# Kernel tuning notes

Measured on AMD Instinct MI355X. Metric: run time of the kernel, lower is better.

Reference implementation:

```python
import jax, jax.numpy as jnp
import numpy as np

EPS = 1e-8
TEMP = 0.1
D, H = 512, 256  # hidden_dim, hidden_dim // 2
BI, R = 64, 36   # images, regions
BC, W = 64, 50   # captions, words


def _l2norm(x):
    n = jnp.linalg.norm(x, axis=-1, keepdims=True)
    return x / jnp.maximum(n, 1e-12)


def _gate(x, w1, b1, w2, b2):
    h = jax.nn.relu(x @ w1 + b1)
    return jax.nn.sigmoid(h @ w2 + b2)  # [..., 1]


def setup_inputs() -> dict:
    key = jax.random.key(0)
    ks = jax.random.split(key, 12)
    imgs = jax.random.normal(ks[0], (BI, R, D), dtype=jnp.float32)
    caps = jax.random.normal(ks[1], (BC, W, D), dtype=jnp.float32)
    img_lens = jax.random.randint(ks[2], (BI,), 1, R + 1).at[0].set(R).astype(jnp.int32)
    cap_lens = jax.random.randint(ks[3], (BC,), 1, W + 1).at[0].set(W).astype(jnp.int32)
    s = 0.02
    return {
        'imgs': imgs, 'caps': caps,
        'soft_w1': jax.random.normal(ks[4], (D, H), dtype=jnp.float32) * s,
        'soft_b1': jnp.zeros((H,), dtype=jnp.float32),
        'soft_w2': jax.random.normal(ks[5], (H, 1), dtype=jnp.float32) * s,
        'soft_b2': jnp.zeros((1,), dtype=jnp.float32),
        'hard_w1': jax.random.normal(ks[6], (D, H), dtype=jnp.float32) * s,
        'hard_b1': jnp.zeros((H,), dtype=jnp.float32),
        'hard_w2': jax.random.normal(ks[7], (H, 1), dtype=jnp.float32) * s,
        'hard_b2': jnp.zeros((1,), dtype=jnp.float32),
        'img_lens': img_lens, 'cap_lens': cap_lens,
    }


def reference(imgs, caps, soft_w1, soft_b1, soft_w2, soft_b2,
              hard_w1, hard_b1, hard_w2, hard_b2, img_lens, cap_lens):
    Bi, R_, D_ = imgs.shape
    Bc, W_, _ = caps.shape
    img_mask = jnp.arange(R_)[None, :] < img_lens[:, None]  # [Bi,R]
    cap_mask = jnp.arange(W_)[None, :] < cap_lens[:, None]  # [Bc,W]
    mask = img_mask[:, None, :, None] & cap_mask[None, :, None, :]  # [Bi,Bc,R,W]

    # fine-grained region-word similarities
    sims = jnp.einsum('ird,cwd->icrw', imgs, caps)

    # hard (top-1) attention: argmax over words, one-hot scatter, re-masked
    idx = jnp.argmax(jnp.where(mask, sims, -1.0), axis=-1)  # [Bi,Bc,R]
    hard_attn = jnp.where(mask, jax.nn.one_hot(idx, W_, dtype=sims.dtype), 0.0)

    # soft attention with temperature and mask
    soft = jax.nn.softmax(jnp.where(mask, sims / TEMP, -jnp.inf), axis=-1)
    soft_attn = jnp.where(mask, soft, 0.0)

    hard_wc = jnp.einsum('icrw,cwd->icrd', hard_attn, caps)
    soft_wc = jnp.einsum('icrw,cwd->icrd', soft_attn, caps)

    # per-region learned gates, normalized to sum ~1
    sg = _gate(imgs, soft_w1, soft_b1, soft_w2, soft_b2)  # [Bi,R,1]
    hg = _gate(imgs, hard_w1, hard_b1, hard_w2, hard_b2)  # [Bi,R,1]
    tot = sg + hg + EPS
    sg = (sg / tot)[:, None, :, :]  # [Bi,1,R,1]
    hg = (hg / tot)[:, None, :, :]

    mixed = sg * soft_wc + hg * hard_wc  # [Bi,Bc,R,D]

    # per-pair, per-region cosine similarity
    out = jnp.einsum('ird,icrd->icr', _l2norm(imgs), _l2norm(mixed))
    return jnp.where(img_mask[:, None, :], out, -1.0)  # [Bi,Bc,R]
```

## Files before the change

kernel.cpp:

```cpp
#include <hip/hip_runtime.h>
#include <math.h>

#define BI 64
#define RR 36
#define BC 64
#define WW 50
#define DD 512
#define HH 256
#define CST 132

typedef _Float16 f16x8 __attribute__((ext_vector_type(8)));
typedef _Float16 f16x4 __attribute__((ext_vector_type(4)));
typedef float    f32x4 __attribute__((ext_vector_type(4)));

__device__ __forceinline__ float wave_sum(float v){
  #pragma unroll
  for (int off=32; off>0; off>>=1) v += __shfl_xor(v, off, 64);
  return v;
}
__device__ __forceinline__ float wave_max(float v){
  #pragma unroll
  for (int off=32; off>0; off>>=1) v = fmaxf(v, __shfl_xor(v, off, 64));
  return v;
}

__device__ __forceinline__ void gl_lds16(const _Float16* g, _Float16* l){
  __builtin_amdgcn_global_load_lds(
      (const __attribute__((address_space(1))) unsigned int*)g,
      (__attribute__((address_space(3))) unsigned int*)l, 16, 0, 0);
}

__global__ __launch_bounds__(256) void prepgram_kernel(
    const float* __restrict__ imgs, const float* __restrict__ caps,
    const float* __restrict__ sw1, const float* __restrict__ hw1,
    _Float16* __restrict__ Ah, _Float16* __restrict__ Al,
    _Float16* __restrict__ Bh, _Float16* __restrict__ Bl,
    float* __restrict__ G, _Float16* __restrict__ Gfrag)
{
  __shared__ __align__(16) float smem[WW*CST + 1024];
  if (blockIdx.x < 1504){
    int u = blockIdx.x*256 + threadIdx.x;
    _Float16 *dh, *dl; int idx;
    if (u < 144*1024){ idx = u;            dh = Ah; dl = Al; }
    else             { idx = u - 144*1024; dh = Bh; dl = Bl; }
    const int tile = idx >> 10, rem = idx & 1023, ks = rem >> 6, lane = rem & 63;
    const int k0 = ks*32 + (lane >> 4)*8;
    f16x8 hv, lv;
    if (u < 144*1024 || tile < 200){
      const float* src = (u < 144*1024) ? imgs : caps;
      const int m = tile*16 + (lane & 15);
      const float* p = src + (size_t)m*DD + k0;
      #pragma unroll
      for (int j=0;j<8;j++){
        float a = p[j];
        _Float16 h = (_Float16)a;
        hv[j] = h;
        lv[j] = (_Float16)((a - (float)h) * 2048.0f);
      }
    } else {
      const int n = (tile-200)*16 + (lane & 15);
      const float* src = (n < HH) ? (sw1 + n) : (hw1 + n - HH);
      #pragma unroll
      for (int j=0;j<8;j++){
        float a = src[(size_t)(k0+j)*HH];
        _Float16 h = (_Float16)a;
        hv[j] = h;
        lv[j] = (_Float16)((a - (float)h) * 2048.0f);
      }
    }
    *(f16x8*)(dh + (size_t)idx*8) = hv;
    *(f16x8*)(dl + (size_t)idx*8) = lv;
  } else {
    float* cs = smem;
    float* Gt = smem + WW*CST;
    const int bxg  = blockIdx.x - 1504;
    const int c    = bxg >> 2;
    const int tile = bxg & 3;
    const int w0   = tile*16;
    const int nw   = (tile==3) ? 2 : 16;
    const int t=threadIdx.x, lane=t&63, wv=t>>6;
    const int wl = lane < WW ? lane : WW-1;
    float acc[4]={0.f,0.f,0.f,0.f};
    for (int k0=0;k0<DD;k0+=128){
      __syncthreads();
      for (int n=t;n<WW*32;n+=256){
        int row=n>>5, c4=(n&31)*4;
        *(float4*)&cs[row*CST+c4] = *(const float4*)(caps + ((size_t)c*WW+row)*DD + k0 + c4);
      }
      __syncthreads();
      for (int k=0;k<128;k+=4){
        float4 cv = *(const float4*)&cs[wl*CST+k];
        #pragma unroll
        for (int q=0;q<4;q++){
          int lw = wv + q*4;
          if (lw < nw){
            float4 bv = *(const float4*)&cs[(w0+lw)*CST+k];
            acc[q]=fmaf(bv.x,cv.x,acc[q]); acc[q]=fmaf(bv.y,cv.y,acc[q]);
            acc[q]=fmaf(bv.z,cv.z,acc[q]); acc[q]=fmaf(bv.w,cv.w,acc[q]);
          }
        }
      }
    }
    for (int n=t;n<1024;n+=256) Gt[n]=0.f;
    __syncthreads();
    if (lane < WW){
      #pragma unroll
      for (int q=0;q<4;q++){
        int lw = wv + q*4;
        if (lw < nw){
          G[(size_t)c*WW*WW + (w0+lw)*WW + lane] = acc[q];
          Gt[lw*64 + lane] = acc[q];
        }
      }
    }
    __syncthreads();
    {
      int flat = t*4;
      int ks = flat>>9, L=(flat>>3)&63, j0=flat&7;
      const bool ones = (tile==3) && ((L&15)==2);
      f16x4 v;
      #pragma unroll
      for (int e=0;e<4;e++)
        v[e] = ones ? (_Float16)1.0f
                    : (_Float16)Gt[(L&15)*64 + ks*32 + ((L>>4)<<3) + j0 + e];
      *(f16x4*)&Gfrag[(size_t)c*4096 + (tile*2+ks)*512 + L*8 + j0] = v;
    }
  }
}

__global__ __launch_bounds__(256, 2) void sgemm_hgate_kernel(
    const _Float16* __restrict__ Ah, const _Float16* __restrict__ Al,
    const _Float16* __restrict__ Bh, const _Float16* __restrict__ Bl,
    float* __restrict__ Sp,
    const float* __restrict__ imgs,
    const float* __restrict__ sb1, const float* __restrict__ hb1,
    const float* __restrict__ sw2, const float* __restrict__ hw2,
    float* __restrict__ drawS, float* __restrict__ drawH,
    float* __restrict__ rnraw)
{
  __shared__ _Float16 lds[2*16384];
  const int t = threadIdx.x, lane = t & 63, wv = t >> 6;

  if (blockIdx.x >= 36){
    const int bx = blockIdx.x - 36;
    const int mb = bx % 18, nb = bx / 18;
    const int wm = wv & 1, wn = wv >> 1;

    f32x4 P[4][4], Q[4][4];
    #pragma unroll
    for (int a=0;a<4;a++)
      #pragma unroll
      for (int b=0;b<4;b++){ P[a][b]=(f32x4){0,0,0,0}; Q[a][b]=(f32x4){0,0,0,0}; }

    const _Float16* sbase = (wv==0)?Ah:(wv==1)?Al:(wv==2)?Bh:Bl;
    const size_t gtb = (size_t)((wv<2)? mb : nb)*8;
    _Float16* buf0 = lds + wv*4096;
    _Float16* buf1 = lds + 16384 + wv*4096;

    #pragma unroll
    for (int s=0;s<8;s++)
      gl_lds16(sbase + (((gtb+s)*16 + 0)*64 + lane)*8, buf0 + s*512);
    asm volatile("s_waitcnt vmcnt(0)" ::: "memory");
    __syncthreads();

    for (int ks=0; ks<16; ks++){
      if (ks < 15){
        _Float16* nb_ = ((ks+1) & 1) ? buf1 : buf0;
        #pragma unroll
        for (int s=0;s<8;s++)
          gl_lds16(sbase + (((gtb+s)*16 + (ks+1))*64 + lane)*8, nb_ + s*512);
      }

      const _Float16* L = lds + (ks & 1)*16384;
      f16x8 a_h[4], a_l[4], b_h[4], b_l[4];
      #pragma unroll
      for (int x=0;x<4;x++){
        a_h[x] = *(const f16x8*)&L[        (wm*4+x)*512 + lane*8];
        a_l[x] = *(const f16x8*)&L[ 4096 + (wm*4+x)*512 + lane*8];
        b_h[x] = *(const f16x8*)&L[ 8192 + (wn*4+x)*512 + lane*8];
        b_l[x] = *(const f16x8*)&L[12288 + (wn*4+x)*512 + lane*8];
      }
      #pragma unroll
      for (int mi=0;mi<4;mi++)
        #pragma unroll
        for (int ni=0;ni<4;ni++){
          P[mi][ni] = __builtin_amdgcn_mfma_f32_16x16x32_f16(a_h[mi], b_h[ni], P[mi][ni],0,0,0);
          Q[mi][ni] = __builtin_amdgcn_mfma_f32_16x16x32_f16(a_h[mi], b_l[ni], Q[mi][ni],0,0,0);
          Q[mi][ni] = __builtin_amdgcn_mfma_f32_16x16x32_f16(a_l[mi], b_h[ni], Q[mi][ni],0,0,0);
        }

      if (ks < 15)
        asm volatile("s_waitcnt vmcnt(0)" ::: "memory");
      __syncthreads();
    }

    const int r0 = mb*128 + wm*64 + ((lane>>4)<<2);
    const int c0 = nb*128 + wn*64 + (lane&15);
    size_t pr[16]; size_t pc[4];
    #pragma unroll
    for (int mi=0;mi<4;mi++)
      #pragma unroll
      for (int reg=0;reg<4;reg++){
        unsigned row = (unsigned)(r0 + mi*16 + reg);
        unsigned i = row / 36u, rr_ = row - i*36u;
        pr[mi*4+reg] = (size_t)i*115200u + (size_t)rr_*50u;
      }
    #pragma unroll
    for (int ni=0;ni<4;ni++){
      unsigned col = (unsigned)(c0 + ni*16);
      unsigned cc = col / 50u, w = col - cc*50u;
      pc[ni] = (size_t)cc*1800u + w;
    }
    #pragma unroll
    for (int mi=0;mi<4;mi++)
      #pragma unroll
      for (int ni=0;ni<4;ni++)
        #pragma unroll
        for (int reg=0;reg<4;reg++)
          Sp[pr[mi*4+reg] + pc[ni]] =
              P[mi][ni][reg] + Q[mi][ni][reg]*(1.0f/2048.0f);
    return;
  }

  const int mb = blockIdx.x >> 1;
  const int br = blockIdx.x & 1;
  const int wm = wv & 1, wn = wv >> 1;

  f32x4 P[4][8];
  #pragma unroll
  for (int a=0;a<4;a++)
    #pragma unroll
    for (int b=0;b<8;b++) P[a][b]=(f32x4){0,0,0,0};

  const _Float16* Bbase = Bh + (size_t)(200 + br*16)*8192;

  #pragma unroll
  for (int s=0;s<6;s++){
    const int u = wv*6 + s;
    const _Float16* src = (u < 8)
      ? (Ah    + ((size_t)((mb*8 + u)*16 + 0)*64 + lane)*8)
      : (Bbase + ((size_t)((u-8)  *16 + 0)*64 + lane)*8);
    _Float16* dst = (u < 8) ? (lds + u*512) : (lds + 4096 + (u-8)*512);
    gl_lds16(src, dst);
  }
  asm volatile("s_waitcnt vmcnt(0)" ::: "memory");
  __syncthreads();

  for (int ks=0; ks<16; ks++){
    if (ks < 15){
      _Float16* buf = lds + (((ks+1) & 1) ? 16384 : 0);
      #pragma unroll
      for (int s=0;s<6;s++){
        const int u = wv*6 + s;
        const _Float16* src = (u < 8)
          ? (Ah    + ((size_t)((mb*8 + u)*16 + (ks+1))*64 + lane)*8)
          : (Bbase + ((size_t)((u-8)  *16 + (ks+1))*64 + lane)*8);
        _Float16* dst = (u < 8) ? (buf + u*512) : (buf + 4096 + (u-8)*512);
        gl_lds16(src, dst);
      }
    }

    const _Float16* L = lds + (ks & 1)*16384;
    f16x8 a[4], b[8];
    #pragma unroll
    for (int x=0;x<4;x++)
      a[x] = *(const f16x8*)&L[(wm*4+x)*512 + lane*8];
    #pragma unroll
    for (int y=0;y<8;y++)
      b[y] = *(const f16x8*)&L[4096 + (wn*8+y)*512 + lane*8];
    #pragma unroll
    for (int mi=0;mi<4;mi++)
      #pragma unroll
      for (int ni=0;ni<8;ni++)
        P[mi][ni] = __builtin_amdgcn_mfma_f32_16x16x32_f16(a[mi], b[ni], P[mi][ni],0,0,0);

    if (ks < 15)
      asm volatile("s_waitcnt vmcnt(0)" ::: "memory");
    __syncthreads();
  }

  const float* b1 = br ? hb1 : sb1;
  const float* w2 = br ? hw2 : sw2;
  float bvv[8], wvv[8];
  #pragma unroll
  for (int ni=0;ni<8;ni++){
    const int cb = wn*128 + ni*16 + (lane&15);
    bvv[ni] = b1[cb]; wvv[ni] = w2[cb];
  }
  float contrib[16];
  #pragma unroll
  for (int mi=0;mi<4;mi++)
    #pragma unroll
    for (int reg=0;reg<4;reg++){
      float cacc = 0.f;
      #pragma unroll
      for (int ni=0;ni<8;ni++)
        cacc = fmaf(fmaxf(P[mi][ni][reg] + bvv[ni], 0.f), wvv[ni], cacc);
      #pragma unroll
      for (int off=1; off<16; off<<=1) cacc += __shfl_xor(cacc, off, 64);
      contrib[mi*4+reg] = cacc;
    }

  float* red = (float*)lds;
  if ((lane & 15) == 0){
    const int rbase = wm*64 + ((lane>>4)<<2);
    #pragma unroll
    for (int mi=0;mi<4;mi++)
      #pragma unroll
      for (int reg=0;reg<4;reg++)
        red[wn*128 + rbase + mi*16 + reg] = contrib[mi*4+reg];
  }
  __syncthreads();
  if (t < 128){
    float draw = red[t] + red[128 + t];
    (br ? drawH : drawS)[mb*128 + t] = draw;
  }

  if (br == 0){
    const int row = mb*128 + (t >> 1);
    const float* p = imgs + (size_t)row*DD + (t & 1)*256;
    float ss = 0.f;
    #pragma unroll
    for (int q=0;q<64;q++){
      float4 x = ((const float4*)p)[q];
      ss += x.x*x.x + x.y*x.y + x.z*x.z + x.w*x.w;
    }
    ss += __shfl_xor(ss, 1, 64);
    if ((t & 1) == 0) rnraw[row] = ss;
  }
}

__global__ __launch_bounds__(512) void epi_kernel(
    const float* __restrict__ Sp,
    const int* __restrict__ img_lens, const int* __restrict__ cap_lens,
    const float* __restrict__ drawS, const float* __restrict__ drawH,
    const float* __restrict__ rnraw,
    const float* __restrict__ G, const _Float16* __restrict__ Gfrag,
    const float* __restrict__ sb2, const float* __restrict__ hb2,
    float* __restrict__ out)
{
  __shared__ __align__(16) _Float16 sEp[48*72];
  __shared__ __align__(16) _Float16 sE2[48*72];
  __shared__ __align__(16) _Float16 sFp[48*72];
  __shared__ __align__(16) _Float16 sGf[4096];
  __shared__ float sTd[48];
  __shared__ float sTS[48];
  __shared__ float sGd[64];
  __shared__ float sAv[40];
  __shared__ int   sAi[40];

  const int bx = blockIdx.x;
  const int i = bx >> 6, c = bx & 63;
  const int t = threadIdx.x, lane = t & 63;
  const int wv = __builtin_amdgcn_readfirstlane(t >> 6);
  const int cap_len = cap_lens[c];
  const int img_len = img_lens[i];

  ((int4*)sGf)[t] = ((const int4*)(Gfrag + (size_t)c*4096))[t];
  if (t < WW) sGd[t] = G[(size_t)c*WW*WW + t*(WW+1)];

  const int r0 = wv*5;
  const float* srow = Sp + (size_t)(i*64 + c)*1800u + (size_t)r0*50;
  float sv[5];
  #pragma unroll
  for (int j=0;j<5;j++)
    sv[j] = ((r0+j) < RR && lane < WW) ? srow[j*50 + lane] : 0.f;

  #pragma unroll
  for (int j=0;j<5;j++){
    const int r = r0 + j;
    const float s = sv[j];
    const bool valid = (lane < cap_len);
    float av = wave_max(valid ? s : -INFINITY);
    unsigned long long m = __ballot(valid && (s == av));
    int ai = (int)(__ffsll((long long)m) - 1);
    float e = valid ? __expf(10.0f*(s - av)) : 0.f;
    sEp[r*72 + lane] = (_Float16)e;
    sE2[r*72 + lane] = (_Float16)(e * s);
    if (lane == 0){ sAv[r] = av; sAi[r] = ai; }
  }
  __syncthreads();

  {
    int mi = wv % 3, nt = wv / 3;
    f32x4 acc = (f32x4){0,0,0,0};
    #pragma unroll
    for (int ks=0; ks<2; ks++){
      f16x8 a = *(const f16x8*)&sEp[(mi*16+(lane&15))*72 + ks*32 + ((lane>>4)<<3)];
      f16x8 b = *(const f16x8*)&sGf[(nt*2+ks)*512 + lane*8];
      acc = __builtin_amdgcn_mfma_f32_16x16x32_f16(a, b, acc, 0,0,0);
    }
    #pragma unroll
    for (int reg=0; reg<4; reg++){
      int row = mi*16 + ((lane>>4)<<2) + reg;
      sFp[row*72 + nt*16 + (lane&15)] = (_Float16)acc[reg];
    }
  }
  if (wv < 4){
    int tau = 8 + wv, mi = tau % 3, nt = tau / 3;
    f32x4 acc = (f32x4){0,0,0,0};
    #pragma unroll
    for (int ks=0; ks<2; ks++){
      f16x8 a = *(const f16x8*)&sEp[(mi*16+(lane&15))*72 + ks*32 + ((lane>>4)<<3)];
      f16x8 b = *(const f16x8*)&sGf[(nt*2+ks)*512 + lane*8];
      acc = __builtin_amdgcn_mfma_f32_16x16x32_f16(a, b, acc, 0,0,0);
    }
    #pragma unroll
    for (int reg=0; reg<4; reg++){
      int row = mi*16 + ((lane>>4)<<2) + reg;
      sFp[row*72 + nt*16 + (lane&15)] = (_Float16)acc[reg];
    }
  } else if (wv < 7){
    int mi = wv - 4;
    f32x4 acc = (f32x4){0,0,0,0};
    #pragma unroll
    for (int ks=0; ks<2; ks++){
      f16x8 a = *(const f16x8*)&sE2[(mi*16+(lane&15))*72 + ks*32 + ((lane>>4)<<3)];
      f16x8 b = *(const f16x8*)&sGf[(3*2+ks)*512 + lane*8];
      acc = __builtin_amdgcn_mfma_f32_16x16x32_f16(a, b, acc, 0,0,0);
    }
    if ((lane & 15) == 2){
      #pragma unroll
      for (int reg=0; reg<4; reg++)
        sTS[mi*16 + ((lane>>4)<<2) + reg] = acc[reg];
    }
  }
  __syncthreads();

  if (wv < 3){
    f32x4 acc = (f32x4){0,0,0,0};
    #pragma unroll
    for (int ks=0; ks<2; ks++){
      f16x8 aF = *(const f16x8*)&sFp[(wv*16+(lane&15))*72 + ks*32 + ((lane>>4)<<3)];
      f16x8 bE = *(const f16x8*)&sEp[(wv*16+(lane&15))*72 + ks*32 + ((lane>>4)<<3)];
      acc = __builtin_amdgcn_mfma_f32_16x16x32_f16(aF, bE, acc, 0,0,0);
    }
    #pragma unroll
    for (int reg=0; reg<4; reg++){
      int row = ((lane>>4)<<2) + reg;
      if (row == (lane&15)) sTd[wv*16 + row] = acc[reg];
    }
  }
  __syncthreads();

  if (wv == 0 && lane < RR){
    const int r = lane;
    const int ai = sAi[r];
    const float av = sAv[r];
    float tQ  = sTd[r];
    float tS  = sTS[r];
    float den = (float)sFp[r*72 + 50];
    float dh  = (float)sFp[r*72 + ai];
    float hh  = sGd[ai];
    float hv  = (av > -1.0f) ? 1.f : 0.f;

    const int rg = i*RR + r;
    float sg_ = 1.f/(1.f+__expf(-(drawS[rg] + sb2[0])));
    float hg_ = 1.f/(1.f+__expf(-(drawH[rg] + hb2[0])));
    float tot = sg_ + hg_ + 1e-8f;
    float gs = sg_/tot, gh = hg_/tot;
    float rx = 1.f/fmaxf(sqrtf(rnraw[rg]), 1e-12f);
    float rd = 1.f/den;
    float num = gs*(tS*rd) + hv*gh*av;
    float n2  = gs*gs*(tQ*rd*rd) + hv*(2.f*gs*gh*(dh*rd) + gh*gh*hh);
    float ov  = num * rx / fmaxf(sqrtf(fmaxf(n2, 0.f)), 1e-12f);
    out[((size_t)i*BC + c)*RR + r] = (r < img_len) ? ov : -1.0f;
  }
}

__global__ __launch_bounds__(256) void gates_kernel(
    const float* __restrict__ imgs,
    const float* __restrict__ sw1, const float* __restrict__ sb1,
    const float* __restrict__ sw2, const float* __restrict__ sb2,
    const float* __restrict__ hw1, const float* __restrict__ hb1,
    const float* __restrict__ hw2, const float* __restrict__ hb2,
    float* __restrict__ sgn, float* __restrict__ hgn, float* __restrict__ rn)
{
  __shared__ __align__(16) float xs[8*DD];
  __shared__ float red[16*256];
  __shared__ float nr[8];
  const int t = threadIdx.x;
  const int row0 = blockIdx.x * 8;
  if (t < 8) nr[t] = 0.f;
  __syncthreads();
  const float4* src = (const float4*)(imgs + (size_t)row0*DD);
  #pragma unroll
  for (int m=0;m<4;m++){
    int n = m*256+t;
    float4 v = src[n];
    ((float4*)xs)[n] = v;
    float ss = v.x*v.x+v.y*v.y+v.z*v.z+v.w*v.w;
    atomicAdd(&nr[n>>7], ss);
  }
  __syncthreads();
  float accS[8]={0,0,0,0,0,0,0,0};
  float accH[8]={0,0,0,0,0,0,0,0};
  for (int k=0;k<DD;k+=4){
    float a0=sw1[(k+0)*HH+t], a1=sw1[(k+1)*HH+t], a2=sw1[(k+2)*HH+t], a3=sw1[(k+3)*HH+t];
    float b0=hw1[(k+0)*HH+t], b1=hw1[(k+1)*HH+t], b2=hw1[(k+2)*HH+t], b3=hw1[(k+3)*HH+t];
    #pragma unroll
    for (int r=0;r<8;r++){
      float4 x = *(const float4*)&xs[r*DD+k];
      accS[r]=fmaf(x.x,a0,accS[r]); accS[r]=fmaf(x.y,a1,accS[r]);
      accS[r]=fmaf(x.z,a2,accS[r]); accS[r]=fmaf(x.w,a3,accS[r]);
      accH[r]=fmaf(x.x,b0,accH[r]); accH[r]=fmaf(x.y,b1,accH[r]);
      accH[r]=fmaf(x.z,b2,accH[r]); accH[r]=fmaf(x.w,b3,accH[r]);
    }
  }
  const float b1s=sb1[t], b1h=hb1[t], w2s=sw2[t], w2h=hw2[t];
  #pragma unroll
  for (int r=0;r<8;r++){
    red[r*256+t]     = w2s * fmaxf(accS[r]+b1s, 0.f);
    red[(8+r)*256+t] = w2h * fmaxf(accH[r]+b1h, 0.f);
  }
  __syncthreads();
  const int wv=t>>6, ln=t&63;
  #pragma unroll
  for (int q=0;q<4;q++){
    int rr_ = wv*4+q;
    float v = red[rr_*256+ln]+red[rr_*256+ln+64]+red[rr_*256+ln+128]+red[rr_*256+ln+192];
    v = wave_sum(v);
    if (ln==0) red[rr_*256] = v;
  }
  __syncthreads();
  if (t<8){
    float os = red[t*256] + sb2[0];
    float oh = red[(8+t)*256] + hb2[0];
    float s = 1.f/(1.f+__expf(-os));
    float h = 1.f/(1.f+__expf(-oh));
    float tot = s+h+1e-8f;
    sgn[row0+t] = s/tot;
    hgn[row0+t] = h/tot;
    rn[row0+t]  = 1.f/fmaxf(sqrtf(nr[t]), 1e-12f);
  }
}

__global__ __launch_bounds__(256) void gram_fb_kernel(
    const float* __restrict__ caps, float* __restrict__ G)
{
  __shared__ __align__(16) float cs[WW*CST];
  const int c    = blockIdx.x >> 2;
  const int tile = blockIdx.x & 3;
  const int w0   = tile*13;
  const int nw   = (tile==3) ? 11 : 13;
  const int t=threadIdx.x, lane=t&63, wv=t>>6;
  const int wl = lane < WW ? lane : WW-1;
  float acc[4]={0.f,0.f,0.f,0.f};
  for (int k0=0;k0<DD;k0+=128){
    __syncthreads();
    for (int n=t;n<WW*32;n+=256){
      int row=n>>5, c4=(n&31)*4;
      *(float4*)&cs[row*CST+c4] = *(const float4*)(caps + ((size_t)c*WW+row)*DD + k0 + c4);
    }
    __syncthreads();
    for (int k=0;k<128;k+=4){
      float4 cv = *(const float4*)&cs[wl*CST+k];
      #pragma unroll
      for (int q=0;q<4;q++){
        int lw = wv + q*4;
        if (lw < nw){
          float4 bv = *(const float4*)&cs[(w0+lw)*CST+k];
          acc[q]=fmaf(bv.x,cv.x,acc[q]); acc[q]=fmaf(bv.y,cv.y,acc[q]);
          acc[q]=fmaf(bv.z,cv.z,acc[q]); acc[q]=fmaf(bv.w,cv.w,acc[q]);
        }
      }
    }
  }
  if (lane < WW){
    #pragma unroll
    for (int q=0;q<4;q++){
      int lw = wv + q*4;
      if (lw < nw) G[(size_t)c*WW*WW + (w0+lw)*WW + lane] = acc[q];
    }
  }
}

__global__ __launch_bounds__(256) void pair_kernel(
    const float* __restrict__ imgs, const float* __restrict__ caps,
    const int* __restrict__ img_lens, const int* __restrict__ cap_lens,
    const float* __restrict__ sgn, const float* __restrict__ hgn,
    const float* __restrict__ rn,
    const float* __restrict__ G, float* __restrict__ out)
{
  __shared__ __align__(16) float smem[WW*CST + 52*52 + RR*52];
  float* cs = smem;
  float* Gs = smem + WW*CST;
  float* As = Gs + 52*52;
  const int bx = blockIdx.x;
  const int i = bx >> 6, c = bx & 63;
  const int t = threadIdx.x, lane = t&63;
  const int wv = __builtin_amdgcn_readfirstlane(t>>6);
  const int wl = lane < WW ? lane : WW-1;
  const int cap_len = cap_lens[c];
  const int img_len = img_lens[i];
  for (int n=t;n<52*52;n+=256){
    int w=n/52, w2=n-w*52;
    Gs[n] = (w<WW && w2<WW) ? G[(size_t)c*WW*WW + w*WW + w2] : 0.f;
  }
  float acc[9]={0,0,0,0,0,0,0,0,0};
  const float* ib = imgs + ((size_t)i*RR + wv*9)*DD;
  for (int k0=0;k0<DD;k0+=128){
    __syncthreads();
    for (int n=t;n<WW*32;n+=256){
      int row=n>>5, c4=(n&31)*4;
      *(float4*)&cs[row*CST+c4] = *(const float4*)(caps + ((size_t)c*WW+row)*DD + k0 + c4);
    }
    __syncthreads();
    for (int k=0;k<128;k+=4){
      float4 cv = *(const float4*)&cs[wl*CST+k];
      #pragma unroll
      for (int j=0;j<9;j++){
        float4 iv = *(const float4*)(ib + j*DD + k0 + k);
        acc[j]=fmaf(iv.x,cv.x,acc[j]); acc[j]=fmaf(iv.y,cv.y,acc[j]);
        acc[j]=fmaf(iv.z,cv.z,acc[j]); acc[j]=fmaf(iv.w,cv.w,acc[j]);
      }
    }
  }
  for (int j=0;j<9;j++){
    const int r = wv*9 + j;
    const float s = acc[j];
    float av; int ai;
    if (lane < cap_len){ av = s;     ai = lane; }
    else if (lane < WW){ av = -1.0f; ai = lane; }
    else               { av = -INFINITY; ai = 64; }
    #pragma unroll
    for (int off=32; off>0; off>>=1){
      float ov = __shfl_xor(av, off, 64);
      int   oi = __shfl_xor(ai, off, 64);
      if (ov > av || (ov == av && oi < ai)){ av = ov; ai = oi; }
    }
    float zv = (lane < cap_len) ? s*10.0f : -INFINITY;
    float zm = wave_max(zv);
    float e  = (lane < cap_len) ? __expf(zv - zm) : 0.f;
    float den = wave_sum(e);
    if (lane < 52) As[r*52 + lane] = (lane < WW) ? e : 0.f;
    float m = 0.f;
    #pragma unroll
    for (int g=0; g<13; g++){
      float4 ab = *(const float4*)&As[r*52 + g*4];
      m = fmaf(ab.x, Gs[(g*4+0)*52+wl], m);
      m = fmaf(ab.y, Gs[(g*4+1)*52+wl], m);
      m = fmaf(ab.z, Gs[(g*4+2)*52+wl], m);
      m = fmaf(ab.w, Gs[(g*4+3)*52+wl], m);
    }
    float tS = wave_sum(e * s);
    float tQ = wave_sum(e * m);
    float dh = __shfl(m, ai, 64);
    float hh = Gs[ai*52 + ai];
    float hv = (ai < cap_len) ? 1.f : 0.f;
    const int rg = i*RR + r;
    float gs = sgn[rg], gh = hgn[rg], rx = rn[rg];
    float rd = 1.f/den;
    float num = gs*(tS*rd) + hv*gh*av;
    float n2  = gs*gs*(tQ*rd*rd) + hv*(2.f*gs*gh*(dh*rd) + gh*gh*hh);
    float ov  = num * rx / fmaxf(sqrtf(fmaxf(n2, 0.f)), 1e-12f);
    if (lane==0) out[((size_t)i*BC + c)*RR + r] = (r < img_len) ? ov : -1.0f;
  }
}

extern "C" void kernel_launch(void* const* d_in, const int* in_sizes, int n_in,
                              void* d_out, int out_size, void* d_ws, size_t ws_size,
                              hipStream_t stream)
{
  const float* imgs = (const float*)d_in[0];
  const float* caps = (const float*)d_in[1];
  const float* sw1  = (const float*)d_in[2];
  const float* sb1  = (const float*)d_in[3];
  const float* sw2  = (const float*)d_in[4];
  const float* sb2  = (const float*)d_in[5];
  const float* hw1  = (const float*)d_in[6];
  const float* hb1  = (const float*)d_in[7];
  const float* hw2  = (const float*)d_in[8];
  const float* hb2  = (const float*)d_in[9];
  const int* img_lens = (const int*)d_in[10];
  const int* cap_lens = (const int*)d_in[11];

  char* base = (char*)d_ws;
  float*    drawS = (float*)(base + 0);
  float*    drawH = (float*)(base + 9216);
  float*    rnraw = (float*)(base + 18432);
  float*    G     = (float*)(base + 27648);
  _Float16* Gfrag = (_Float16*)(base + 667648);
  _Float16* Ah    = (_Float16*)(base + 1191936);
  _Float16* Al    = (_Float16*)(base + 3551232);
  _Float16* Bh    = (_Float16*)(base + 5910528);
  _Float16* Bl    = (_Float16*)(base + 9711616);
  float*    Sp    = (float*)(base + 18231296);
  const size_t NEED = 47722496ull;

  float* out = (float*)d_out;

  if (ws_size >= NEED){
    hipLaunchKernelGGL(prepgram_kernel, dim3(1760), dim3(256), 0, stream,
                       imgs, caps, sw1, hw1, Ah, Al, Bh, Bl, G, Gfrag);
    hipLaunchKernelGGL(sgemm_hgate_kernel, dim3(486), dim3(256), 0, stream,
                       Ah, Al, Bh, Bl, Sp,
                       imgs, sb1, hb1, sw2, hw2, drawS, drawH, rnraw);
    hipLaunchKernelGGL(epi_kernel, dim3(BI*BC), dim3(512), 0, stream,
                       Sp, img_lens, cap_lens, drawS, drawH, rnraw,
                       G, Gfrag, sb2, hb2, out);
  } else {
    hipLaunchKernelGGL(gates_kernel, dim3(288), dim3(256), 0, stream,
                       imgs, sw1, sb1, sw2, sb2, hw1, hb1, hw2, hb2,
                       drawS, drawH, rnraw);
    hipLaunchKernelGGL(gram_fb_kernel, dim3(256), dim3(256), 0, stream, caps, G);
    hipLaunchKernelGGL(pair_kernel, dim3(BI*BC), dim3(256), 0, stream,
                       imgs, caps, img_lens, cap_lens, drawS, drawH, rnraw, G, out);
  }
}
```

Measured before the change: 173.7 us.

## Switch similarity and gate GEMMs to 32x32x16 MFMA with deeper LDS pipeline

Repacks the split-fp16 operand fragments into a 32-row by 16-k layout and rewrites both GEMM paths to use 32x32x16 MFMA instructions instead of 16x16x32. The similarity GEMM now uses a four-buffer LDS ring with three k-steps of prefetch and partial vmcnt waits, replacing the double buffer that waited for every load. The gate GEMM uses the new fragment layout and reduces across 32 lanes in its epilogue. The aim is fewer LDS reads per MFMA and better overlap of loads with compute, at the cost of more complex indexing and different accumulator register pressure.

```diff
diff --git a/kernel.cpp b/kernel.cpp
--- a/kernel.cpp
+++ b/kernel.cpp
@@ -12,6 +12,7 @@
 typedef _Float16 f16x8 __attribute__((ext_vector_type(8)));
 typedef _Float16 f16x4 __attribute__((ext_vector_type(4)));
 typedef float    f32x4 __attribute__((ext_vector_type(4)));
+typedef float    f32x16 __attribute__((ext_vector_type(16)));
 
 __device__ __forceinline__ float wave_sum(float v){
   #pragma unroll
@@ -43,12 +44,13 @@
     _Float16 *dh, *dl; int idx;
     if (u < 144*1024){ idx = u;            dh = Ah; dl = Al; }
     else             { idx = u - 144*1024; dh = Bh; dl = Bl; }
-    const int tile = idx >> 10, rem = idx & 1023, ks = rem >> 6, lane = rem & 63;
-    const int k0 = ks*32 + (lane >> 4)*8;
+    const int frag = idx >> 6, lane = idx & 63;
+    const int t32 = frag >> 5, kk = frag & 31;
+    const int k0 = kk*16 + (lane >> 5)*8;
     f16x8 hv, lv;
-    if (u < 144*1024 || tile < 200){
+    if (u < 144*1024 || t32 < 100){
       const float* src = (u < 144*1024) ? imgs : caps;
-      const int m = tile*16 + (lane & 15);
+      const int m = t32*32 + (lane & 31);
       const float* p = src + (size_t)m*DD + k0;
       #pragma unroll
       for (int j=0;j<8;j++){
@@ -58,7 +60,7 @@
         lv[j] = (_Float16)((a - (float)h) * 2048.0f);
       }
     } else {
-      const int n = (tile-200)*16 + (lane & 15);
+      const int n = (t32-100)*32 + (lane & 31);
       const float* src = (n < HH) ? (sw1 + n) : (hw1 + n - HH);
       #pragma unroll
       for (int j=0;j<8;j++){
@@ -138,7 +140,7 @@
     float* __restrict__ drawS, float* __restrict__ drawH,
     float* __restrict__ rnraw)
 {
-  __shared__ _Float16 lds[2*16384];
+  __shared__ _Float16 lds[4*8192];
   const int t = threadIdx.x, lane = t & 63, wv = t >> 6;
 
   if (blockIdx.x >= 36){
@@ -146,79 +148,88 @@
     const int mb = bx % 18, nb = bx / 18;
     const int wm = wv & 1, wn = wv >> 1;
 
-    f32x4 P[4][4], Q[4][4];
-    #pragma unroll
-    for (int a=0;a<4;a++)
-      #pragma unroll
-      for (int b=0;b<4;b++){ P[a][b]=(f32x4){0,0,0,0}; Q[a][b]=(f32x4){0,0,0,0}; }
-
-    const _Float16* sbase = (wv==0)?Ah:(wv==1)?Al:(wv==2)?Bh:Bl;
-    const size_t gtb = (size_t)((wv<2)? mb : nb)*8;
-    _Float16* buf0 = lds + wv*4096;
-    _Float16* buf1 = lds + 16384 + wv*4096;
-
-    #pragma unroll
-    for (int s=0;s<8;s++)
-      gl_lds16(sbase + (((gtb+s)*16 + 0)*64 + lane)*8, buf0 + s*512);
+    f32x16 P[2][2], Q[2][2];
+    #pragma unroll
+    for (int a=0;a<2;a++)
+      #pragma unroll
+      for (int b=0;b<2;b++){
+        #pragma unroll
+        for (int e=0;e<16;e++){ P[a][b][e]=0.f; Q[a][b][e]=0.f; }
+      }
+
+    const _Float16* mybase = (wv==0)?Ah:(wv==1)?Al:(wv==2)?Bh:Bl;
+    const size_t fb4 = (size_t)((wv<2)? mb : nb)*4;
+
+    auto sg_stage = [&](int kk, int bufi){
+      _Float16* dstb = lds + bufi*8192 + (wv*4)*512;
+      const _Float16* sp_ = mybase + ((fb4*32 + (size_t)kk)*64 + lane)*8;
+      #pragma unroll
+      for (int s=0;s<4;s++)
+        gl_lds16(sp_ + (size_t)s*16384, dstb + s*512);
+    };
+    auto sg_compute = [&](int bufi){
+      const _Float16* L = lds + bufi*8192;
+      f16x8 a_h[2], a_l[2], b_h[2], b_l[2];
+      #pragma unroll
+      for (int rb=0;rb<2;rb++){
+        a_h[rb] = *(const f16x8*)&L[(     wm*2+rb)*512 + lane*8];
+        a_l[rb] = *(const f16x8*)&L[( 4 + wm*2+rb)*512 + lane*8];
+      }
+      #pragma unroll
+      for (int cb=0;cb<2;cb++){
+        b_h[cb] = *(const f16x8*)&L[( 8 + wn*2+cb)*512 + lane*8];
+        b_l[cb] = *(const f16x8*)&L[(12 + wn*2+cb)*512 + lane*8];
+      }
+      asm volatile("s_waitcnt lgkmcnt(0)" ::: "memory");
+      __builtin_amdgcn_sched_barrier(0);
+      #pragma unroll
+      for (int rb=0;rb<2;rb++)
+        #pragma unroll
+        for (int cb=0;cb<2;cb++){
+          P[rb][cb] = __builtin_amdgcn_mfma_f32_32x32x16_f16(a_h[rb], b_h[cb], P[rb][cb],0,0,0);
+          Q[rb][cb] = __builtin_amdgcn_mfma_f32_32x32x16_f16(a_h[rb], b_l[cb], Q[rb][cb],0,0,0);
+          Q[rb][cb] = __builtin_amdgcn_mfma_f32_32x32x16_f16(a_l[rb], b_h[cb], Q[rb][cb],0,0,0);
+        }
+    };
+
+    sg_stage(0,0); sg_stage(1,1); sg_stage(2,2);
+
+    for (int kk=0; kk<30; kk++){
+      asm volatile("s_waitcnt vmcnt(8)" ::: "memory");
+      __builtin_amdgcn_s_barrier();
+      asm volatile("" ::: "memory");
+      if (kk < 29) sg_stage(kk+3, (kk+3)&3);
+      sg_compute(kk&3);
+    }
+    asm volatile("s_waitcnt vmcnt(4)" ::: "memory");
+    __builtin_amdgcn_s_barrier();
+    asm volatile("" ::: "memory");
+    sg_compute(30&3);
     asm volatile("s_waitcnt vmcnt(0)" ::: "memory");
-    __syncthreads();
-
-    for (int ks=0; ks<16; ks++){
-      if (ks < 15){
-        _Float16* nb_ = ((ks+1) & 1) ? buf1 : buf0;
+    __builtin_amdgcn_s_barrier();
+    asm volatile("" ::: "memory");
+    sg_compute(31&3);
+
+    const unsigned colbase = (unsigned)(nb*128 + wn*64 + (lane&31));
+    unsigned pc[2];
+    #pragma unroll
+    for (int cb=0;cb<2;cb++){
+      unsigned col = colbase + cb*32;
+      unsigned cc = col / 50u, w = col - cc*50u;
+      pc[cb] = cc*1800u + w;
+    }
+    const unsigned rowbase = (unsigned)(mb*128 + wm*64 + ((lane>>5)<<2));
+    #pragma unroll
+    for (int rb=0;rb<2;rb++)
+      #pragma unroll
+      for (int reg=0;reg<16;reg++){
+        unsigned row = rowbase + rb*32 + (reg&3) + 8*(reg>>2);
+        unsigned i = row / 36u, rr_ = row - i*36u;
+        size_t pr = (size_t)i*115200u + (size_t)rr_*50u;
         #pragma unroll
-        for (int s=0;s<8;s++)
-          gl_lds16(sbase + (((gtb+s)*16 + (ks+1))*64 + lane)*8, nb_ + s*512);
-      }
-
-      const _Float16* L = lds + (ks & 1)*16384;
-      f16x8 a_h[4], a_l[4], b_h[4], b_l[4];
-      #pragma unroll
-      for (int x=0;x<4;x++){
-        a_h[x] = *(const f16x8*)&L[        (wm*4+x)*512 + lane*8];
-        a_l[x] = *(const f16x8*)&L[ 4096 + (wm*4+x)*512 + lane*8];
-        b_h[x] = *(const f16x8*)&L[ 8192 + (wn*4+x)*512 + lane*8];
-        b_l[x] = *(const f16x8*)&L[12288 + (wn*4+x)*512 + lane*8];
-      }
-      #pragma unroll
-      for (int mi=0;mi<4;mi++)
-        #pragma unroll
-        for (int ni=0;ni<4;ni++){
-          P[mi][ni] = __builtin_amdgcn_mfma_f32_16x16x32_f16(a_h[mi], b_h[ni], P[mi][ni],0,0,0);
-          Q[mi][ni] = __builtin_amdgcn_mfma_f32_16x16x32_f16(a_h[mi], b_l[ni], Q[mi][ni],0,0,0);
-          Q[mi][ni] = __builtin_amdgcn_mfma_f32_16x16x32_f16(a_l[mi], b_h[ni], Q[mi][ni],0,0,0);
-        }
-
-      if (ks < 15)
-        asm volatile("s_waitcnt vmcnt(0)" ::: "memory");
-      __syncthreads();
-    }
-
-    const int r0 = mb*128 + wm*64 + ((lane>>4)<<2);
-    const int c0 = nb*128 + wn*64 + (lane&15);
-    size_t pr[16]; size_t pc[4];
-    #pragma unroll
-    for (int mi=0;mi<4;mi++)
-      #pragma unroll
-      for (int reg=0;reg<4;reg++){
-        unsigned row = (unsigned)(r0 + mi*16 + reg);
-        unsigned i = row / 36u, rr_ = row - i*36u;
-        pr[mi*4+reg] = (size_t)i*115200u + (size_t)rr_*50u;
-      }
-    #pragma unroll
-    for (int ni=0;ni<4;ni++){
-      unsigned col = (unsigned)(c0 + ni*16);
-      unsigned cc = col / 50u, w = col - cc*50u;
-      pc[ni] = (size_t)cc*1800u + w;
-    }
-    #pragma unroll
-    for (int mi=0;mi<4;mi++)
-      #pragma unroll
-      for (int ni=0;ni<4;ni++)
-        #pragma unroll
-        for (int reg=0;reg<4;reg++)
-          Sp[pr[mi*4+reg] + pc[ni]] =
-              P[mi][ni][reg] + Q[mi][ni][reg]*(1.0f/2048.0f);
+        for (int cb=0;cb<2;cb++)
+          Sp[pr + pc[cb]] = P[rb][cb][reg] + Q[rb][cb][reg]*(1.0f/2048.0f);
+      }
     return;
   }
 
@@ -226,90 +237,78 @@
   const int br = blockIdx.x & 1;
   const int wm = wv & 1, wn = wv >> 1;
 
-  f32x4 P[4][8];
-  #pragma unroll
-  for (int a=0;a<4;a++)
-    #pragma unroll
-    for (int b=0;b<8;b++) P[a][b]=(f32x4){0,0,0,0};
-
-  const _Float16* Bbase = Bh + (size_t)(200 + br*16)*8192;
-
-  #pragma unroll
-  for (int s=0;s<6;s++){
-    const int u = wv*6 + s;
-    const _Float16* src = (u < 8)
-      ? (Ah    + ((size_t)((mb*8 + u)*16 + 0)*64 + lane)*8)
-      : (Bbase + ((size_t)((u-8)  *16 + 0)*64 + lane)*8);
-    _Float16* dst = (u < 8) ? (lds + u*512) : (lds + 4096 + (u-8)*512);
-    gl_lds16(src, dst);
-  }
-  asm volatile("s_waitcnt vmcnt(0)" ::: "memory");
-  __syncthreads();
-
+  f32x16 Acc[2][4];
+  #pragma unroll
+  for (int a=0;a<2;a++)
+    #pragma unroll
+    for (int b=0;b<4;b++){
+      #pragma unroll
+      for (int e=0;e<16;e++) Acc[a][b][e]=0.f;
+    }
+
+  auto hg_stage = [&](int ks, int bufi){
+    #pragma unroll
+    for (int s=0;s<6;s++){
+      const int u = wv*6 + s;
+      const int h = (u >= 12) ? 1 : 0, uu = u - h*12;
+      const size_t frag = (uu < 4)
+        ? (size_t)((mb*4 + uu)*32 + ks*2 + h)
+        : (size_t)((100 + br*8 + (uu-4))*32 + ks*2 + h);
+      const _Float16* src = ((uu < 4) ? Ah : Bh) + (frag*64 + lane)*8;
+      gl_lds16(src, lds + bufi*12288 + h*6144 + uu*512);
+    }
+  };
+  auto hg_compute = [&](int bufi){
+    const _Float16* Lb = lds + bufi*12288;
+    #pragma unroll
+    for (int h=0;h<2;h++){
+      f16x8 a[2], b[4];
+      #pragma unroll
+      for (int rb=0;rb<2;rb++)
+        a[rb] = *(const f16x8*)&Lb[h*6144 + (wm*2+rb)*512 + lane*8];
+      #pragma unroll
+      for (int cb=0;cb<4;cb++)
+        b[cb] = *(const f16x8*)&Lb[h*6144 + (4 + wn*4 + cb)*512 + lane*8];
+      #pragma unroll
+      for (int rb=0;rb<2;rb++)
+        #pragma unroll
+        for (int cb=0;cb<4;cb++)
+          Acc[rb][cb] = __builtin_amdgcn_mfma_f32_32x32x16_f16(a[rb], b[cb], Acc[rb][cb],0,0,0);
+    }
+  };
+
+  hg_stage(0,0);
+  __syncthreads();
   for (int ks=0; ks<16; ks++){
-    if (ks < 15){
-      _Float16* buf = lds + (((ks+1) & 1) ? 16384 : 0);
-      #pragma unroll
-      for (int s=0;s<6;s++){
-        const int u = wv*6 + s;
-        const _Float16* src = (u < 8)
-          ? (Ah    + ((size_t)((mb*8 + u)*16 + (ks+1))*64 + lane)*8)
-          : (Bbase + ((size_t)((u-8)  *16 + (ks+1))*64 + lane)*8);
-        _Float16* dst = (u < 8) ? (buf + u*512) : (buf + 4096 + (u-8)*512);
-        gl_lds16(src, dst);
-      }
-    }
-
-    const _Float16* L = lds + (ks & 1)*16384;
-    f16x8 a[4], b[8];
-    #pragma unroll
-    for (int x=0;x<4;x++)
-      a[x] = *(const f16x8*)&L[(wm*4+x)*512 + lane*8];
-    #pragma unroll
-    for (int y=0;y<8;y++)
-      b[y] = *(const f16x8*)&L[4096 + (wn*8+y)*512 + lane*8];
-    #pragma unroll
-    for (int mi=0;mi<4;mi++)
-      #pragma unroll
-      for (int ni=0;ni<8;ni++)
-        P[mi][ni] = __builtin_amdgcn_mfma_f32_16x16x32_f16(a[mi], b[ni], P[mi][ni],0,0,0);
-
-    if (ks < 15)
-      asm volatile("s_waitcnt vmcnt(0)" ::: "memory");
+    if (ks < 15) hg_stage(ks+1, (ks+1)&1);
+    hg_compute(ks&1);
     __syncthreads();
   }
 
   const float* b1 = br ? hb1 : sb1;
   const float* w2 = br ? hw2 : sw2;
-  float bvv[8], wvv[8];
-  #pragma unroll
-  for (int ni=0;ni<8;ni++){
-    const int cb = wn*128 + ni*16 + (lane&15);
-    bvv[ni] = b1[cb]; wvv[ni] = w2[cb];
-  }
-  float contrib[16];
-  #pragma unroll
-  for (int mi=0;mi<4;mi++)
-    #pragma unroll
-    for (int reg=0;reg<4;reg++){
+  float bvv[4], wvv[4];
+  #pragma unroll
+  for (int cb=0;cb<4;cb++){
+    const int col = wn*128 + cb*32 + (lane&31);
+    bvv[cb] = b1[col]; wvv[cb] = w2[col];
+  }
+  float* red = (float*)lds;
+  #pragma unroll
+  for (int rb=0;rb<2;rb++)
+    #pragma unroll
+    for (int reg=0;reg<16;reg++){
       float cacc = 0.f;
       #pragma unroll
-      for (int ni=0;ni<8;ni++)
-        cacc = fmaf(fmaxf(P[mi][ni][reg] + bvv[ni], 0.f), wvv[ni], cacc);
-      #pragma unroll
-      for (int off=1; off<16; off<<=1) cacc += __shfl_xor(cacc, off, 64);
-      contrib[mi*4+reg] = cacc;
-    }
-
-  float* red = (float*)lds;
-  if ((lane & 15) == 0){
-    const int rbase = wm*64 + ((lane>>4)<<2);
-    #pragma unroll
-    for (int mi=0;mi<4;mi++)
-      #pragma unroll
-      for (int reg=0;reg<4;reg++)
-        red[wn*128 + rbase + mi*16 + reg] = contrib[mi*4+reg];
-  }
+      for (int cb=0;cb<4;cb++)
+        cacc = fmaf(fmaxf(Acc[rb][cb][reg] + bvv[cb], 0.f), wvv[cb], cacc);
+      #pragma unroll
+      for (int off=1; off<32; off<<=1) cacc += __shfl_xor(cacc, off, 64);
+      if ((lane & 31) == 0){
+        const int row = wm*64 + rb*32 + (reg&3) + 8*(reg>>2) + ((lane>>5)<<2);
+        red[wn*128 + row] = cacc;
+      }
+    }
   __syncthreads();
   if (t < 128){
     float draw = red[t] + red[128 + t];
```

Result: slower. 178.2 us (+2.6%).

## Compute caption Gram matrix with split-fp16 MFMA, one block per caption

Applied to the files above, without the earlier changes.

The caption Gram matrix was computed with scalar FP32 FMAs from LDS-staged tiles, using four blocks per caption. It now uses one block per caption, with four waves each computing a 32x32 tile via 32x32x16 f16 MFMA. A hi/lo fp16 split with three MFMAs per step approximates FP32 accuracy. This removes LDS staging and most scalar FMA work and cuts the grid by 192 blocks, at the cost of slightly different numerics.

```diff
diff --git a/kernel.cpp b/kernel.cpp
--- a/kernel.cpp
+++ b/kernel.cpp
@@ -12,6 +12,7 @@
 typedef _Float16 f16x8 __attribute__((ext_vector_type(8)));
 typedef _Float16 f16x4 __attribute__((ext_vector_type(4)));
 typedef float    f32x4 __attribute__((ext_vector_type(4)));
+typedef float    f32x16 __attribute__((ext_vector_type(16)));
 
 __device__ __forceinline__ float wave_sum(float v){
   #pragma unroll
@@ -37,7 +38,7 @@
     _Float16* __restrict__ Bh, _Float16* __restrict__ Bl,
     float* __restrict__ G, _Float16* __restrict__ Gfrag)
 {
-  __shared__ __align__(16) float smem[WW*CST + 1024];
+  __shared__ __align__(16) float smem[64*64];
   if (blockIdx.x < 1504){
     int u = blockIdx.x*256 + threadIdx.x;
     _Float16 *dh, *dl; int idx;
@@ -71,59 +72,68 @@
     *(f16x8*)(dh + (size_t)idx*8) = hv;
     *(f16x8*)(dl + (size_t)idx*8) = lv;
   } else {
-    float* cs = smem;
-    float* Gt = smem + WW*CST;
-    const int bxg  = blockIdx.x - 1504;
-    const int c    = bxg >> 2;
-    const int tile = bxg & 3;
-    const int w0   = tile*16;
-    const int nw   = (tile==3) ? 2 : 16;
-    const int t=threadIdx.x, lane=t&63, wv=t>>6;
-    const int wl = lane < WW ? lane : WW-1;
-    float acc[4]={0.f,0.f,0.f,0.f};
-    for (int k0=0;k0<DD;k0+=128){
-      __syncthreads();
-      for (int n=t;n<WW*32;n+=256){
-        int row=n>>5, c4=(n&31)*4;
-        *(float4*)&cs[row*CST+c4] = *(const float4*)(caps + ((size_t)c*WW+row)*DD + k0 + c4);
-      }
-      __syncthreads();
-      for (int k=0;k<128;k+=4){
-        float4 cv = *(const float4*)&cs[wl*CST+k];
-        #pragma unroll
-        for (int q=0;q<4;q++){
-          int lw = wv + q*4;
-          if (lw < nw){
-            float4 bv = *(const float4*)&cs[(w0+lw)*CST+k];
-            acc[q]=fmaf(bv.x,cv.x,acc[q]); acc[q]=fmaf(bv.y,cv.y,acc[q]);
-            acc[q]=fmaf(bv.z,cv.z,acc[q]); acc[q]=fmaf(bv.w,cv.w,acc[q]);
-          }
-        }
-      }
-    }
-    for (int n=t;n<1024;n+=256) Gt[n]=0.f;
+    float* Gt = smem;
+    const int c = blockIdx.x - 1504;
+    const int t = threadIdx.x, lane = t & 63, wv = t >> 6;
+    const int wm = wv & 1, wn = wv >> 1;
+    const float* cbase = caps + (size_t)c*WW*DD;
+
+    f32x16 P, Q;
+    #pragma unroll
+    for (int e=0;e<16;e++){ P[e]=0.f; Q[e]=0.f; }
+
+    const int r  = lane & 31;
+    const int k8 = (lane >> 5)*8;
+    const int wA = wm*32 + r;
+    const int wB = wn*32 + r;
+    const float* pA = cbase + (size_t)wA*DD + k8;
+    const float* pB = cbase + (size_t)wB*DD + k8;
+
+    for (int ks=0; ks<32; ks++){
+      const int k0 = ks*16;
+      float4 a0, a1, b0, b1;
+      if (wA < WW){ a0 = *(const float4*)(pA + k0); a1 = *(const float4*)(pA + k0 + 4); }
+      else        { a0 = (float4){0,0,0,0}; a1 = a0; }
+      if (wB < WW){ b0 = *(const float4*)(pB + k0); b1 = *(const float4*)(pB + k0 + 4); }
+      else        { b0 = (float4){0,0,0,0}; b1 = b0; }
+      float av[8] = {a0.x,a0.y,a0.z,a0.w,a1.x,a1.y,a1.z,a1.w};
+      float bw[8] = {b0.x,b0.y,b0.z,b0.w,b1.x,b1.y,b1.z,b1.w};
+      f16x8 ah, al, bh, bl;
+      #pragma unroll
+      for (int j=0;j<8;j++){
+        _Float16 h = (_Float16)av[j];
+        ah[j] = h; al[j] = (_Float16)((av[j]-(float)h)*2048.0f);
+        _Float16 g = (_Float16)bw[j];
+        bh[j] = g; bl[j] = (_Float16)((bw[j]-(float)g)*2048.0f);
+      }
+      P = __builtin_amdgcn_mfma_f32_32x32x16_f16(ah, bh, P,0,0,0);
+      Q = __builtin_amdgcn_mfma_f32_32x32x16_f16(ah, bl, Q,0,0,0);
+      Q = __builtin_amdgcn_mfma_f32_32x32x16_f16(al, bh, Q,0,0,0);
+    }
+
+    const int col = wn*32 + (lane & 31);
+    #pragma unroll
+    for (int reg=0; reg<16; reg++){
+      const int row = wm*32 + (reg&3) + 8*(reg>>2) + 4*(lane>>5);
+      float g = P[reg] + Q[reg]*(1.0f/2048.0f);
+      Gt[row*64 + col] = g;
+      if (row < WW && col < WW)
+        G[(size_t)c*WW*WW + row*WW + col] = g;
+    }
     __syncthreads();
-    if (lane < WW){
-      #pragma unroll
-      for (int q=0;q<4;q++){
-        int lw = wv + q*4;
-        if (lw < nw){
-          G[(size_t)c*WW*WW + (w0+lw)*WW + lane] = acc[q];
-          Gt[lw*64 + lane] = acc[q];
-        }
-      }
-    }
-    __syncthreads();
-    {
+
+    #pragma unroll
+    for (int tile=0; tile<4; tile++){
       int flat = t*4;
-      int ks = flat>>9, L=(flat>>3)&63, j0=flat&7;
+      int ks2 = flat>>9, L=(flat>>3)&63, j0=flat&7;
       const bool ones = (tile==3) && ((L&15)==2);
+      int n  = tile*16 + (L&15);
+      int kk = ks2*32 + ((L>>4)<<3) + j0;
       f16x4 v;
       #pragma unroll
       for (int e=0;e<4;e++)
-        v[e] = ones ? (_Float16)1.0f
-                    : (_Float16)Gt[(L&15)*64 + ks*32 + ((L>>4)<<3) + j0 + e];
-      *(f16x4*)&Gfrag[(size_t)c*4096 + (tile*2+ks)*512 + L*8 + j0] = v;
+        v[e] = ones ? (_Float16)1.0f : (_Float16)Gt[n*64 + kk + e];
+      *(f16x4*)&Gfrag[(size_t)c*4096 + (tile*2+ks2)*512 + L*8 + j0] = v;
     }
   }
 }
@@ -691,7 +701,7 @@
   float* out = (float*)d_out;
 
   if (ws_size >= NEED){
-    hipLaunchKernelGGL(prepgram_kernel, dim3(1760), dim3(256), 0, stream,
+    hipLaunchKernelGGL(prepgram_kernel, dim3(1568), dim3(256), 0, stream,
                        imgs, caps, sw1, hw1, Ah, Al, Bh, Bl, G, Gfrag);
     hipLaunchKernelGGL(sgemm_hgate_kernel, dim3(486), dim3(256), 0, stream,
                        Ah, Al, Bh, Bl, Sp,
```

Measured after the change: 154.8 us. 1.12x faster.
